# Optimization experiments

Hardware: AMD Instinct MI355X
Metric: run time of the kernel (lower is better)

The kernel has to match this reference:

```python
import jax, jax.numpy as jnp
import numpy as np

B, N, L = 8, 128, 32


def setup_inputs() -> dict:
    key = jax.random.key(0)
    k1, k2 = jax.random.split(key)
    # probabilities in (0,1); clamp away from exact 0/1 to keep log finite
    inp = jax.random.uniform(k1, (B, N, N, L, L), dtype=jnp.float32,
                             minval=1e-6, maxval=1.0 - 1e-6)
    tgt = jax.random.randint(k2, (B, N, N, L), 0, 2, dtype=jnp.int32)
    return {"input": inp, "target": tgt}


def reference(input, target):
    b, n, _, l, _ = input.shape
    g = target.astype(input.dtype)                      # [B,N,N,L] in {0,1}
    diag = jnp.einsum('bijkk->bijk', input)             # p = input[...,k,k]
    # faithful to: -log(p**g * (1-p)**(1-g))
    ce = -jnp.log(diag ** g * (1.0 - diag) ** (1.0 - g))  # [B,N,N,L]
    offdiag = (1.0 - jnp.eye(n, dtype=input.dtype))[None, :, :, None]  # skip i==j
    num = float(n * (n - 1) * l)
    loss = jnp.sum(ce * offdiag) / num / float(b)
    # accuracy: diag element is the max of its row <=> predicted positive
    is_max = diag == jnp.max(input, axis=-1)            # [B,N,N,L] bool
    correct = jnp.where(g == 1.0, is_max, ~is_max)      # per-label correctness
    offb = offdiag > 0
    single_acc = jnp.sum((correct & offb).astype(jnp.float32)) / (b * n * (n - 1) * l)
    multi = jnp.all(correct, axis=-1, keepdims=True)    # all labels right for pair
    multi_acc = jnp.sum((multi & offb).astype(jnp.float32)) / (b * n * (n - 1))
    return (loss, single_acc, multi_acc)
```

## Files before the change

kernel.cpp:

```cpp
#include <hip/hip_runtime.h>


#define BB 8
#define NN 128
#define LL 32
#define NPAIRS (BB * NN * NN)
#define NWAVES 8192
#define PPW (NPAIRS / NWAVES)
#define PF 2
#define NCHUNK (PPW / PF)

__global__ void fsmre_init_ws(float* ws) {
    if (threadIdx.x < 3) ws[threadIdx.x] = 0.0f;
}

__global__ __launch_bounds__(256, 4) void fsmre_main(const float* __restrict__ input,
                                                     const int* __restrict__ target,
                                                     float* __restrict__ ws) {
    const int lane = threadIdx.x & 63;
    const int grp  = lane >> 3;
    const int sub  = lane & 7;
    const int comp = grp & 3;

    const int waveId = blockIdx.x * (blockDim.x >> 6) + (threadIdx.x >> 6);
    const int P0 = waveId * PPW;

    float acc_ce = 0.0f, acc_single = 0.0f, acc_multi = 0.0f;

    for (int c = 0; c < NCHUNK; ++c) {
        const int Pa = P0 + c * PF;

        float4 q[PF][4];
        int    tq[PF][4];
        #pragma unroll
        for (int p = 0; p < PF; ++p) {
            const float4* __restrict__ bp = (const float4*)input + (long long)(Pa + p) * (LL * LL / 4);
            #pragma unroll
            for (int v = 0; v < 4; ++v) q[p][v] = bp[v * 64 + lane];
            const int* __restrict__ tb = target + (long long)(Pa + p) * LL;
            #pragma unroll
            for (int v = 0; v < 4; ++v) tq[p][v] = tb[v * 8 + grp];
        }

        #pragma unroll
        for (int p = 0; p < PF; ++p) {
            const int P  = Pa + p;
            const int ij = P & (NN * NN - 1);
            const bool offd = ((ij >> 7) != (ij & (NN - 1)));

            bool all_ok = true;
            float ce = 0.0f;
            int single = 0;

            #pragma unroll
            for (int v = 0; v < 4; ++v) {
                const float4 qq = q[p][v];
                float m = fmaxf(fmaxf(qq.x, qq.y), fmaxf(qq.z, qq.w));
                m = fmaxf(m, __shfl_xor(m, 1, 64));
                m = fmaxf(m, __shfl_xor(m, 2, 64));
                m = fmaxf(m, __shfl_xor(m, 4, 64));

                const float pd = (comp == 0) ? qq.x : (comp == 1) ? qq.y : (comp == 2) ? qq.z : qq.w;
                const bool holder = (sub == 2 * v + (grp >> 2));
                const int  t = tq[p][v];
                const bool is_max = (pd == m);
                const bool okr = t ? is_max : !is_max;

                const float val = holder ? (t ? pd : 1.0f - pd) : 1.0f;
                ce -= __logf(val);
                single += (holder && okr) ? 1 : 0;
                all_ok &= (!holder) || okr;
            }

            if (offd) {
                acc_ce += ce;
                acc_single += (float)single;
                if (__all(all_ok) && lane == 0) acc_multi += 1.0f;
            }
        }
    }

    #pragma unroll
    for (int d = 1; d < 64; d <<= 1) {
        acc_ce     += __shfl_xor(acc_ce, d, 64);
        acc_single += __shfl_xor(acc_single, d, 64);
        acc_multi  += __shfl_xor(acc_multi, d, 64);
    }
    if (lane == 0) {
        atomicAdd(&ws[0], acc_ce);
        atomicAdd(&ws[1], acc_single);
        atomicAdd(&ws[2], acc_multi);
    }
}

__global__ void fsmre_finalize(const float* __restrict__ ws, float* __restrict__ out) {
    if (threadIdx.x == 0) {
        const double pairs = (double)BB * NN * (NN - 1);
        out[0] = (float)((double)ws[0] / ((double)NN * (NN - 1) * LL) / (double)BB);
        out[1] = (float)((double)ws[1] / (pairs * LL));
        out[2] = (float)((double)ws[2] / pairs);
    }
}

extern "C" void kernel_launch(void* const* d_in, const int* in_sizes, int n_in,
                              void* d_out, int out_size, void* d_ws, size_t ws_size,
                              hipStream_t stream) {
    const float* input  = (const float*)d_in[0];
    const int*   target = (const int*)d_in[1];
    float* out = (float*)d_out;
    float* ws  = (float*)d_ws;

    fsmre_init_ws<<<1, 64, 0, stream>>>(ws);
    fsmre_main<<<NWAVES / 4, 256, 0, stream>>>(input, target, ws);
    fsmre_finalize<<<1, 64, 0, stream>>>(ws, out);
}
```

Baseline: 921.3 us.

## Stream input pairs through per-wave LDS double buffer via direct global-to-LDS loads

Replaces direct per-lane float4 register loads of each pair's 32x32 tile with `global_load_lds` 16-byte transfers into a per-wave double-buffered shared-memory region. The next chunk is prefetched while the current one is processed. The grid shrinks to 512 blocks (2048 waves) with launch bounds lowered to 2, so each wave handles more pairs. The goal is to hide global memory latency and cut register pressure. The trade-offs: the unconditional `s_waitcnt vmcnt(0)` also waits on the prefetch just issued, which limits the overlap, and the smaller grid lowers the number of waves in flight per CU.

```diff
diff --git a/kernel.cpp b/kernel.cpp
--- a/kernel.cpp
+++ b/kernel.cpp
@@ -1,52 +1,88 @@
 #include <hip/hip_runtime.h>
+#include <stdint.h>
 
 
 #define BB 8
 #define NN 128
 #define LL 32
 #define NPAIRS (BB * NN * NN)
-#define NWAVES 8192
+#define NBLOCKS 512
+#define WPB 4
+#define NWAVES (NBLOCKS * WPB)
 #define PPW (NPAIRS / NWAVES)
 #define PF 2
 #define NCHUNK (PPW / PF)
+#define PAIR_FLOATS (LL * LL)
+#define CHUNK_FLOATS (PF * PAIR_FLOATS)
 
 __global__ void fsmre_init_ws(float* ws) {
     if (threadIdx.x < 3) ws[threadIdx.x] = 0.0f;
 }
 
-__global__ __launch_bounds__(256, 4) void fsmre_main(const float* __restrict__ input,
+__device__ __forceinline__ void gll16(const float* g, float* l) {
+#if __has_builtin(__builtin_amdgcn_global_load_lds)
+    auto* lds3 = reinterpret_cast<__attribute__((address_space(3))) uint32_t*>(
+        (uint32_t)(uintptr_t)l);
+    __builtin_amdgcn_global_load_lds(
+        (const __attribute__((address_space(1))) uint32_t*)(const void*)g,
+        lds3, 16, 0, 0);
+#else
+    *(float4*)l = *(const float4*)g;
+#endif
+}
+
+__global__ __launch_bounds__(256, 2) void fsmre_main(const float* __restrict__ input,
                                                      const int* __restrict__ target,
                                                      float* __restrict__ ws) {
+    __shared__ float smem[WPB * 2 * CHUNK_FLOATS];
+
     const int lane = threadIdx.x & 63;
+    const int wib  = threadIdx.x >> 6;
     const int grp  = lane >> 3;
     const int sub  = lane & 7;
     const int comp = grp & 3;
 
-    const int waveId = blockIdx.x * (blockDim.x >> 6) + (threadIdx.x >> 6);
+    const int waveId = blockIdx.x * WPB + wib;
     const int P0 = waveId * PPW;
+
+    float* myLds = smem + wib * (2 * CHUNK_FLOATS);
 
     float acc_ce = 0.0f, acc_single = 0.0f, acc_multi = 0.0f;
 
+    {
+        const float* g0 = input + (long long)P0 * PAIR_FLOATS + lane * 4;
+        float* l0 = myLds + lane * 4;
+        #pragma unroll
+        for (int s = 0; s < PF * 4; ++s) gll16(g0 + s * 256, l0 + s * 256);
+    }
+
     for (int c = 0; c < NCHUNK; ++c) {
-        const int Pa = P0 + c * PF;
+        const int buf = c & 1;
 
-        float4 q[PF][4];
-        int    tq[PF][4];
+        if (c + 1 < NCHUNK) {
+            const float* g0 = input + (long long)(P0 + (c + 1) * PF) * PAIR_FLOATS + lane * 4;
+            float* l0 = myLds + (buf ^ 1) * CHUNK_FLOATS + lane * 4;
+            #pragma unroll
+            for (int s = 0; s < PF * 4; ++s) gll16(g0 + s * 256, l0 + s * 256);
+        }
+
+        int tq[PF][4];
         #pragma unroll
         for (int p = 0; p < PF; ++p) {
-            const float4* __restrict__ bp = (const float4*)input + (long long)(Pa + p) * (LL * LL / 4);
-            #pragma unroll
-            for (int v = 0; v < 4; ++v) q[p][v] = bp[v * 64 + lane];
-            const int* __restrict__ tb = target + (long long)(Pa + p) * LL;
+            const int* __restrict__ tb = target + (long long)(P0 + c * PF + p) * LL;
             #pragma unroll
             for (int v = 0; v < 4; ++v) tq[p][v] = tb[v * 8 + grp];
         }
 
+        asm volatile("s_waitcnt vmcnt(0)" ::: "memory");
+
         #pragma unroll
         for (int p = 0; p < PF; ++p) {
-            const int P  = Pa + p;
+            const int P  = P0 + c * PF + p;
             const int ij = P & (NN * NN - 1);
             const bool offd = ((ij >> 7) != (ij & (NN - 1)));
+
+            const float* lp = myLds + buf * CHUNK_FLOATS + p * PAIR_FLOATS;
 
             bool all_ok = true;
             float ce = 0.0f;
@@ -54,7 +90,8 @@
 
             #pragma unroll
             for (int v = 0; v < 4; ++v) {
-                const float4 qq = q[p][v];
+                const float4 qq = *((const float4*)(lp + v * 256) + lane);
+
                 float m = fmaxf(fmaxf(qq.x, qq.y), fmaxf(qq.z, qq.w));
                 m = fmaxf(m, __shfl_xor(m, 1, 64));
                 m = fmaxf(m, __shfl_xor(m, 2, 64));
@@ -111,6 +148,6 @@
     float* ws  = (float*)d_ws;
 
     fsmre_init_ws<<<1, 64, 0, stream>>>(ws);
-    fsmre_main<<<NWAVES / 4, 256, 0, stream>>>(input, target, ws);
+    fsmre_main<<<NBLOCKS, 256, 0, stream>>>(input, target, ws);
     fsmre_finalize<<<1, 64, 0, stream>>>(ws, out);
 }
```

Result: faster. 757.1 us (-17.8%).
